# Performance work log

Hardware: AMD Instinct MI355X
Metric: run time of the kernel (lower is better)

## Reference

```python
import jax, jax.numpy as jnp
import numpy as np

B, N, D = 4, 4096, 1024       # batch, seq_len, model dim
H, DH = 16, 64                # heads, dim per head
W = 256                       # sliding window size (causal: keys in [i-W+1, i])


def setup_inputs() -> dict:
    key = jax.random.key(0)
    k1, k2, k3 = jax.random.split(key, 3)
    x = jax.random.normal(k1, (B, N, D), dtype=jnp.float32)
    w_qkv = jax.random.normal(k2, (D, 3 * H * DH), dtype=jnp.float32) * (D ** -0.5)
    w_out = jax.random.normal(k3, (H * DH, D), dtype=jnp.float32) * ((H * DH) ** -0.5)
    return {"x": x, "w_qkv": w_qkv, "w_out": w_out}


def _sliding_window_attn(q, k, v):
    """Causal sliding-window attention, banded (block-local) computation.

    q,k,v: [BH, N, DH]; query i attends keys j with i-W+1 <= j <= i.
    Identical math to masking a full NxN score matrix with -finfo.max then softmax.
    """
    BH, n, dh = q.shape
    nb = n // W  # N is a multiple of W
    qb = q.reshape(BH, nb, W, dh)
    pad = jnp.zeros((BH, W, dh), q.dtype)
    kp = jnp.concatenate([pad, k], axis=1).reshape(BH, nb + 1, W, dh)
    vp = jnp.concatenate([pad, v], axis=1).reshape(BH, nb + 1, W, dh)
    # each query block sees previous block + current block of keys -> 2W keys
    kw = jnp.concatenate([kp[:, :-1], kp[:, 1:]], axis=2)  # [BH, nb, 2W, dh]
    vw = jnp.concatenate([vp[:, :-1], vp[:, 1:]], axis=2)
    scores = jnp.einsum('bnqd,bnkd->bnqk', qb, kw)  # [BH, nb, W, 2W]
    blk = jnp.arange(nb)[:, None, None]
    ii = jnp.arange(W)[None, :, None]
    jj = jnp.arange(2 * W)[None, None, :]
    # absolute key index = blk*W + jj - W ; absolute query index = blk*W + ii
    mask = (jj - W <= ii) & (jj >= ii + 1) & (blk * W + jj - W >= 0)
    neg = -jnp.finfo(scores.dtype).max  # matches torch max_neg_value
    scores = jnp.where(mask[None], scores, neg)
    attn = jax.nn.softmax(scores, axis=-1)
    out = jnp.einsum('bnqk,bnkd->bnqd', attn, vw)
    return out.reshape(BH, n, dh)


def reference(x, w_qkv, w_out):
    b, n, d = x.shape
    qkv = x @ w_qkv                      # [b, n, 3*H*DH]
    q, k, v = jnp.split(qkv, 3, axis=-1)

    def to_heads(t):  # b n (h d) -> (b h) n d
        return t.reshape(b, n, H, DH).transpose(0, 2, 1, 3).reshape(b * H, n, DH)

    q, k, v = map(to_heads, (q, k, v))
    q = q * (DH ** -0.5)                 # default scale = dim_head**-0.5
    out = _sliding_window_attn(q, k, v)  # [(b h), n, DH]
    out = out.reshape(b, H, n, DH).transpose(0, 2, 1, 3).reshape(b, n, H * DH)
    return out @ w_out
```

## Files before the change

kernel.cpp:

```cpp
#include <hip/hip_runtime.h>

typedef __attribute__((ext_vector_type(8))) short short8;
typedef __attribute__((ext_vector_type(4))) float floatx4;

#define AS1(p) ((const __attribute__((address_space(1))) void*)(uintptr_t)(p))
#define AS3(p) ((__attribute__((address_space(3))) void*)(unsigned int)(uintptr_t)(p))

__device__ __forceinline__ unsigned short f2bf(float f) {
    union { float f; unsigned int u; } v; v.f = f;
    unsigned int u = v.u;
    unsigned int r = (u + 0x7FFFu + ((u >> 16) & 1u)) >> 16;
    return (unsigned short)r;
}

__device__ __forceinline__ int pk_bf16(float a, float b) {
#if __has_builtin(__builtin_amdgcn_cvt_pk_bf16_f32)
    auto r = __builtin_amdgcn_cvt_pk_bf16_f32(a, b);
    int out; __builtin_memcpy(&out, &r, sizeof(int)); return out;
#else
    return (int)f2bf(a) | ((int)f2bf(b) << 16);
#endif
}

__global__ __launch_bounds__(256) void transpose_bf16(const float* __restrict__ src,
                                                      unsigned short* __restrict__ dst,
                                                      int R, int C) {
    __shared__ float tile[32][33];
    int c0 = blockIdx.x * 32, r0 = blockIdx.y * 32;
    int tc = threadIdx.x & 31, tr = (threadIdx.x >> 5) * 4;
#pragma unroll
    for (int i = 0; i < 4; ++i)
        tile[tr + i][tc] = src[(size_t)(r0 + tr + i) * C + c0 + tc];
    __syncthreads();
#pragma unroll
    for (int i = 0; i < 4; ++i)
        dst[(size_t)(c0 + tr + i) * R + r0 + tc] = f2bf(tile[tc][tr + i]);
}

template <bool OUT_BF16, bool FUSE_A>
__global__ __launch_bounds__(256, 2) void gemm_bt128(const void* __restrict__ Avoid,
                                                     const unsigned short* __restrict__ Bt,
                                                     void* __restrict__ Cout,
                                                     int M, int N, int K, int nbx) {
    __shared__ unsigned short Asm[2][128 * 32];
    __shared__ unsigned short Bsm[2][256 * 32];

    const unsigned short* A16 = (const unsigned short*)Avoid;
    const float* A32 = (const float*)Avoid;

    const int tid = threadIdx.x;
    const int wn = tid >> 6, lane = tid & 63, quad = lane >> 4, l15 = lane & 15;

    const int nwg = (int)gridDim.x;
    const int q8 = nwg >> 3;
    const int wgid = (int)blockIdx.x;
    const int swz = (wgid & 7) * q8 + (wgid >> 3);
    const int bm = (swz / nbx) * 128;
    const int bn = (swz % nbx) * 256;

    floatx4 acc[8][4];
    const floatx4 z = {0.f, 0.f, 0.f, 0.f};
#pragma unroll
    for (int mi = 0; mi < 8; ++mi)
#pragma unroll
        for (int ni = 0; ni < 4; ++ni) acc[mi][ni] = z;

    const int dA0 = tid, dA1 = tid + 256;
    const int rA0 = dA0 >> 2, cA0 = ((dA0 & 3) ^ ((dA0 >> 3) & 3)) * 8;
    const int rA1 = dA1 >> 2, cA1 = ((dA1 & 3) ^ ((dA1 >> 3) & 3)) * 8;
    const unsigned short* Bsrc[4];
    int dB[4];
#pragma unroll
    for (int j = 0; j < 4; ++j) {
        dB[j] = tid + j * 256;
        const int r = dB[j] >> 2, c = ((dB[j] & 3) ^ ((dB[j] >> 3) & 3)) * 8;
        Bsrc[j] = Bt + (size_t)(bn + r) * K + c;
    }

    const int NT = K >> 5;

    auto stageB = [&](int t) {
        const int s = t & 1, ko = t * 32;
#pragma unroll
        for (int j = 0; j < 4; ++j)
            __builtin_amdgcn_global_load_lds(AS1(Bsrc[j] + ko), AS3(&Bsm[s][dB[j] * 8]), 16, 0, 0);
    };
    auto stageA16 = [&](int t) {
        const int s = t & 1, ko = t * 32;
        __builtin_amdgcn_global_load_lds(AS1(A16 + (size_t)(bm + rA0) * K + cA0 + ko),
                                         AS3(&Asm[s][dA0 * 8]), 16, 0, 0);
        __builtin_amdgcn_global_load_lds(AS1(A16 + (size_t)(bm + rA1) * K + cA1 + ko),
                                         AS3(&Asm[s][dA1 * 8]), 16, 0, 0);
    };

    float4 ar0, ar1, ar2, ar3;
    auto loadA32 = [&](int t) {
        const float* p0 = A32 + (size_t)(bm + rA0) * K + cA0 + t * 32;
        const float* p1 = A32 + (size_t)(bm + rA1) * K + cA1 + t * 32;
        ar0 = *(const float4*)p0; ar1 = *(const float4*)(p0 + 4);
        ar2 = *(const float4*)p1; ar3 = *(const float4*)(p1 + 4);
    };
    auto writeA32 = [&](int t) {
        const int s = t & 1;
        int4 w0 = {pk_bf16(ar0.x, ar0.y), pk_bf16(ar0.z, ar0.w),
                   pk_bf16(ar1.x, ar1.y), pk_bf16(ar1.z, ar1.w)};
        int4 w1 = {pk_bf16(ar2.x, ar2.y), pk_bf16(ar2.z, ar2.w),
                   pk_bf16(ar3.x, ar3.y), pk_bf16(ar3.z, ar3.w)};
        *(int4*)&Asm[s][dA0 * 8] = w0;
        *(int4*)&Asm[s][dA1 * 8] = w1;
    };

    const int qc = (quad ^ ((l15 >> 1) & 3)) * 8;
    const int brow = wn * 64 + l15;

    stageB(0);
    if (FUSE_A) { loadA32(0); writeA32(0); } else stageA16(0);
    asm volatile("s_waitcnt vmcnt(0)" ::: "memory");
    if (FUSE_A) asm volatile("s_waitcnt lgkmcnt(0)" ::: "memory");
    __builtin_amdgcn_s_barrier();

    for (int t = 0; t < NT; ++t) {
        const int s = t & 1;
        const unsigned short* Ap = Asm[s];
        const unsigned short* Bp = Bsm[s];
        if (t + 1 < NT) {
            stageB(t + 1);
            if (FUSE_A) loadA32(t + 1); else stageA16(t + 1);
        }

        short8 b[4], a0[4], a1[4];
#pragma unroll
        for (int ni = 0; ni < 4; ++ni)
            b[ni] = *(const short8*)&Bp[(brow + ni * 16) * 32 + qc];
#pragma unroll
        for (int mi = 0; mi < 4; ++mi)
            a0[mi] = *(const short8*)&Ap[(mi * 16 + l15) * 32 + qc];
#pragma unroll
        for (int mi = 0; mi < 4; ++mi)
            a1[mi] = *(const short8*)&Ap[(64 + mi * 16 + l15) * 32 + qc];

        __builtin_amdgcn_s_setprio(1);
#pragma unroll
        for (int mi = 0; mi < 4; ++mi)
#pragma unroll
            for (int ni = 0; ni < 4; ++ni)
                acc[mi][ni] = __builtin_amdgcn_mfma_f32_16x16x32_bf16(b[ni], a0[mi], acc[mi][ni], 0, 0, 0);
#pragma unroll
        for (int mi = 0; mi < 4; ++mi)
#pragma unroll
            for (int ni = 0; ni < 4; ++ni)
                acc[4 + mi][ni] = __builtin_amdgcn_mfma_f32_16x16x32_bf16(b[ni], a1[mi], acc[4 + mi][ni], 0, 0, 0);
        __builtin_amdgcn_s_setprio(0);

        if (FUSE_A && t + 1 < NT) writeA32(t + 1);
        asm volatile("s_waitcnt vmcnt(0)" ::: "memory");
        if (FUSE_A) asm volatile("s_waitcnt lgkmcnt(0)" ::: "memory");
        __builtin_amdgcn_s_barrier();
    }

#pragma unroll
    for (int mi = 0; mi < 8; ++mi) {
        const size_t row = (size_t)(bm + mi * 16 + l15);
#pragma unroll
        for (int ni = 0; ni < 4; ++ni) {
            const size_t col = (size_t)(bn + wn * 64 + ni * 16 + quad * 4);
            if (OUT_BF16) {
                int2 val = {pk_bf16(acc[mi][ni][0], acc[mi][ni][1]),
                            pk_bf16(acc[mi][ni][2], acc[mi][ni][3])};
                *(int2*)((unsigned short*)Cout + row * N + col) = val;
            } else {
                *(float4*)((float*)Cout + row * N + col) = *(const float4*)&acc[mi][ni];
            }
        }
    }
}

__global__ __launch_bounds__(256, 3) void attn_swin(const unsigned short* __restrict__ qkv,
                                                    unsigned short* __restrict__ attn_out) {
    __shared__ unsigned short Klds[2][64 * 72];
    __shared__ unsigned short Vtl[2][64 * 72];

    const int blk = blockIdx.x, bh = blockIdx.y;
    const int b = bh >> 4, h = bh & 15;
    const int tid = threadIdx.x;
    const int wave = tid >> 6, lane = tid & 63, quad = lane >> 4, l15 = lane & 15;
    const int pair = wave >> 1;
    const int qoff = (wave & 1) * 32;
    const int qi_base = blk * 128 + wave * 32;
    const size_t seqbase = (size_t)b * 4096;

    short8 qf[2][2];
#pragma unroll
    for (int qt = 0; qt < 2; ++qt)
#pragma unroll
        for (int ks = 0; ks < 2; ++ks)
            qf[qt][ks] = *(const short8*)(qkv + (seqbase + qi_base + qt * 16 + l15) * 3072
                                          + h * 64 + ks * 32 + quad * 8);

    floatx4 o[2][4];
    const floatx4 z = {0.f, 0.f, 0.f, 0.f};
    float m_run[2], l_run[2];
#pragma unroll
    for (int qt = 0; qt < 2; ++qt) {
#pragma unroll
        for (int dt = 0; dt < 4; ++dt) o[qt][dt] = z;
        m_run[qt] = -1.0e30f; l_run[qt] = 0.f;
    }

    const int kwin0 = blk * 128 - 256;
    const int c0 = (blk >= 2) ? 0 : (4 - 2 * blk);
    const int cLo = pair, cHi = pair + 4;
    const int sk_key = tid >> 2, sk_g = (tid & 3) * 16;
    const int sv_key = tid & 63, sv_dg = (tid >> 6) * 16;
    const float SC = 0.18033688f;

    const int addrA = (((quad & 1) << 5) + l15) << 2;
    const int addrB = addrA + 64;
    const bool hiq = quad >= 2;

    int4 kvreg[4];
    auto load_kv = [&](int k0) {
        const int4* sk = (const int4*)(qkv + (seqbase + k0 + sk_key) * 3072 + 1024 + h * 64 + sk_g);
        kvreg[0] = sk[0]; kvreg[1] = sk[1];
        const int4* sv = (const int4*)(qkv + (seqbase + k0 + sv_key) * 3072 + 2048 + h * 64 + sv_dg);
        kvreg[2] = sv[0]; kvreg[3] = sv[1];
    };
    auto write_kv = [&](int buf) {
        *(int4*)&Klds[buf][sk_key * 72 + sk_g]     = kvreg[0];
        *(int4*)&Klds[buf][sk_key * 72 + sk_g + 8] = kvreg[1];
        union { unsigned short s[16]; int4 q[2]; } t;
        t.q[0] = kvreg[2]; t.q[1] = kvreg[3];
#pragma unroll
        for (int i = 0; i < 16; ++i) Vtl[buf][(sv_dg + i) * 72 + sv_key] = t.s[i];
    };

    load_kv(kwin0 + c0 * 64);
    write_kv(0);

    for (int c = c0; c < 6; ++c) {
        const int buf = (c - c0) & 1;
        __syncthreads();
        if (c < 5) load_kv(kwin0 + (c + 1) * 64);

        if (c >= cLo && c <= cHi) {
            floatx4 sT[2][4];
#pragma unroll
            for (int qt = 0; qt < 2; ++qt)
#pragma unroll
                for (int ni = 0; ni < 4; ++ni) sT[qt][ni] = z;
            __builtin_amdgcn_s_setprio(1);
#pragma unroll
            for (int ks = 0; ks < 2; ++ks) {
#pragma unroll
                for (int ni = 0; ni < 4; ++ni) {
                    short8 kf = *(const short8*)&Klds[buf][(ni * 16 + l15) * 72 + ks * 32 + quad * 8];
                    sT[0][ni] = __builtin_amdgcn_mfma_f32_16x16x32_bf16(kf, qf[0][ks], sT[0][ni], 0, 0, 0);
                    sT[1][ni] = __builtin_amdgcn_mfma_f32_16x16x32_bf16(kf, qf[1][ks], sT[1][ni], 0, 0, 0);
                }
            }
            __builtin_amdgcn_s_setprio(0);

            if (c == cLo) {
#pragma unroll
                for (int qt = 0; qt < 2; ++qt) {
                    const int i64 = qoff + qt * 16 + l15;
#pragma unroll
                    for (int ni = 0; ni < 4; ++ni) {
                        int jb = ni * 16 + quad * 4;
#pragma unroll
                        for (int r = 0; r < 4; ++r)
                            if (jb + r < i64 + 1) sT[qt][ni][r] = -3.0e38f;
                    }
                }
            } else if (c == cHi) {
#pragma unroll
                for (int qt = 0; qt < 2; ++qt) {
                    const int i64 = qoff + qt * 16 + l15;
#pragma unroll
                    for (int ni = 0; ni < 4; ++ni) {
                        int jb = ni * 16 + quad * 4;
#pragma unroll
                        for (int r = 0; r < 4; ++r)
                            if (jb + r > i64) sT[qt][ni][r] = -3.0e38f;
                    }
                }
            }

            float mx[2], mn[2], alpha[2], ls[2];
            int Pk[2][4][2];
#pragma unroll
            for (int qt = 0; qt < 2; ++qt) {
                mx[qt] = -3.0e38f;
#pragma unroll
                for (int ni = 0; ni < 4; ++ni)
#pragma unroll
                    for (int r = 0; r < 4; ++r) mx[qt] = fmaxf(mx[qt], sT[qt][ni][r]);
            }
#pragma unroll
            for (int qt = 0; qt < 2; ++qt) {
                mx[qt] = fmaxf(mx[qt], __shfl_xor(mx[qt], 16));
                mx[qt] = fmaxf(mx[qt], __shfl_xor(mx[qt], 32));
                mn[qt] = fmaxf(m_run[qt], mx[qt] * SC);
                alpha[qt] = __builtin_amdgcn_exp2f(m_run[qt] - mn[qt]);
                m_run[qt] = mn[qt];
                ls[qt] = 0.f;
            }
#pragma unroll
            for (int qt = 0; qt < 2; ++qt) {
#pragma unroll
                for (int ni = 0; ni < 4; ++ni) {
                    float p0 = __builtin_amdgcn_exp2f(fmaf(sT[qt][ni][0], SC, -mn[qt]));
                    float p1 = __builtin_amdgcn_exp2f(fmaf(sT[qt][ni][1], SC, -mn[qt]));
                    float p2 = __builtin_amdgcn_exp2f(fmaf(sT[qt][ni][2], SC, -mn[qt]));
                    float p3 = __builtin_amdgcn_exp2f(fmaf(sT[qt][ni][3], SC, -mn[qt]));
                    ls[qt] += (p0 + p1) + (p2 + p3);
                    Pk[qt][ni][0] = pk_bf16(p0, p1);
                    Pk[qt][ni][1] = pk_bf16(p2, p3);
                }
            }
#pragma unroll
            for (int qt = 0; qt < 2; ++qt) {
                ls[qt] += __shfl_xor(ls[qt], 16);
                ls[qt] += __shfl_xor(ls[qt], 32);
                l_run[qt] = l_run[qt] * alpha[qt] + ls[qt];
#pragma unroll
                for (int dt = 0; dt < 4; ++dt)
#pragma unroll
                    for (int r = 0; r < 4; ++r) o[qt][dt][r] *= alpha[qt];
            }

            short8 vf[4][2];
#pragma unroll
            for (int dt = 0; dt < 4; ++dt)
#pragma unroll
                for (int ks = 0; ks < 2; ++ks)
                    vf[dt][ks] = *(const short8*)&Vtl[buf][(dt * 16 + l15) * 72 + ks * 32 + quad * 8];

#pragma unroll
            for (int qt = 0; qt < 2; ++qt) {
#pragma unroll
                for (int ks = 0; ks < 2; ++ks) {
                    int a0 = __builtin_amdgcn_ds_bpermute(addrA, Pk[qt][2 * ks][0]);
                    int b0 = __builtin_amdgcn_ds_bpermute(addrA, Pk[qt][2 * ks + 1][0]);
                    int a1 = __builtin_amdgcn_ds_bpermute(addrA, Pk[qt][2 * ks][1]);
                    int b1 = __builtin_amdgcn_ds_bpermute(addrA, Pk[qt][2 * ks + 1][1]);
                    int a2 = __builtin_amdgcn_ds_bpermute(addrB, Pk[qt][2 * ks][0]);
                    int b2 = __builtin_amdgcn_ds_bpermute(addrB, Pk[qt][2 * ks + 1][0]);
                    int a3 = __builtin_amdgcn_ds_bpermute(addrB, Pk[qt][2 * ks][1]);
                    int b3 = __builtin_amdgcn_ds_bpermute(addrB, Pk[qt][2 * ks + 1][1]);
                    union { int i[4]; short8 v; } u;
                    u.i[0] = hiq ? b0 : a0;
                    u.i[1] = hiq ? b1 : a1;
                    u.i[2] = hiq ? b2 : a2;
                    u.i[3] = hiq ? b3 : a3;
                    __builtin_amdgcn_s_setprio(1);
#pragma unroll
                    for (int dt = 0; dt < 4; ++dt)
                        o[qt][dt] = __builtin_amdgcn_mfma_f32_16x16x32_bf16(vf[dt][ks], u.v, o[qt][dt], 0, 0, 0);
                    __builtin_amdgcn_s_setprio(0);
                }
            }
        }

        if (c < 5) write_kv(buf ^ 1);
    }

#pragma unroll
    for (int qt = 0; qt < 2; ++qt) {
        float rl = __builtin_amdgcn_rcpf(l_run[qt]);
        size_t rowb = (seqbase + qi_base + qt * 16 + l15) * 1024 + h * 64;
#pragma unroll
        for (int dt = 0; dt < 4; ++dt) {
            int2 val = {pk_bf16(o[qt][dt][0] * rl, o[qt][dt][1] * rl),
                        pk_bf16(o[qt][dt][2] * rl, o[qt][dt][3] * rl)};
            *(int2*)(attn_out + rowb + dt * 16 + quad * 4) = val;
        }
    }
}

extern "C" void kernel_launch(void* const* d_in, const int* in_sizes, int n_in,
                              void* d_out, int out_size, void* d_ws, size_t ws_size,
                              hipStream_t stream) {
    const float* x     = (const float*)d_in[0];
    const float* w_qkv = (const float*)d_in[1];
    const float* w_out = (const float*)d_in[2];
    float* out = (float*)d_out;

    unsigned short* wqkvT = (unsigned short*)d_ws;
    unsigned short* woutT = wqkvT + (size_t)3072 * 1024;
    unsigned short* qkv   = woutT + (size_t)1024 * 1024;
    unsigned short* attn  = qkv   + (size_t)16384 * 3072;

    transpose_bf16<<<dim3(96, 32), 256, 0, stream>>>(w_qkv, wqkvT, 1024, 3072);
    transpose_bf16<<<dim3(32, 32), 256, 0, stream>>>(w_out, woutT, 1024, 1024);
    gemm_bt128<true, true><<<1536, 256, 0, stream>>>((const void*)x, wqkvT, qkv,
                                                     16384, 3072, 1024, 12);
    attn_swin<<<dim3(32, 64), 256, 0, stream>>>(qkv, attn);
    gemm_bt128<false, false><<<512, 256, 0, stream>>>((const void*)attn, woutT, out,
                                                      16384, 1024, 1024, 4);
}
```

Before: 395.3 us.

## Prefetch fp32 A tiles two steps ahead with ping-pong register sets

In the GEMM path that converts fp32 A to bf16 on the fly, A is now loaded into registers two K-tiles ahead, alternating between two register sets. The main loop is unrolled by two so the sets swap roles. Each step converts and writes the next tile to shared memory at the top of the step, before the MFMAs, so the latency of the global loads is hidden behind a full tile of compute. The end-of-step wait uses a partial vmcnt so the in-flight prefetch is not waited on. This adds register pressure and assumes an even tile count.

Result: faster. 381.2 us (-3.6%).

```diff
diff --git a/kernel.cpp b/kernel.cpp
--- a/kernel.cpp
+++ b/kernel.cpp
@@ -93,19 +93,24 @@
                                          AS3(&Asm[s][dA1 * 8]), 16, 0, 0);
     };
 
-    float4 ar0, ar1, ar2, ar3;
-    auto loadA32 = [&](int t) {
-        const float* p0 = A32 + (size_t)(bm + rA0) * K + cA0 + t * 32;
-        const float* p1 = A32 + (size_t)(bm + rA1) * K + cA1 + t * 32;
-        ar0 = *(const float4*)p0; ar1 = *(const float4*)(p0 + 4);
-        ar2 = *(const float4*)p1; ar3 = *(const float4*)(p1 + 4);
-    };
-    auto writeA32 = [&](int t) {
+    const float* As32_0 = FUSE_A ? A32 + (size_t)(bm + rA0) * K + cA0 : nullptr;
+    const float* As32_1 = FUSE_A ? A32 + (size_t)(bm + rA1) * K + cA1 : nullptr;
+    float4 pA0, pA1, pA2, pA3;
+    float4 pB0, pB1, pB2, pB3;
+
+    auto loadA = [&](int t, float4& r0, float4& r1, float4& r2, float4& r3) {
+        const float* p0 = As32_0 + t * 32;
+        const float* p1 = As32_1 + t * 32;
+        r0 = *(const float4*)p0; r1 = *(const float4*)(p0 + 4);
+        r2 = *(const float4*)p1; r3 = *(const float4*)(p1 + 4);
+    };
+    auto writeA = [&](int t, const float4& r0, const float4& r1,
+                      const float4& r2, const float4& r3) {
         const int s = t & 1;
-        int4 w0 = {pk_bf16(ar0.x, ar0.y), pk_bf16(ar0.z, ar0.w),
-                   pk_bf16(ar1.x, ar1.y), pk_bf16(ar1.z, ar1.w)};
-        int4 w1 = {pk_bf16(ar2.x, ar2.y), pk_bf16(ar2.z, ar2.w),
-                   pk_bf16(ar3.x, ar3.y), pk_bf16(ar3.z, ar3.w)};
+        int4 w0 = {pk_bf16(r0.x, r0.y), pk_bf16(r0.z, r0.w),
+                   pk_bf16(r1.x, r1.y), pk_bf16(r1.z, r1.w)};
+        int4 w1 = {pk_bf16(r2.x, r2.y), pk_bf16(r2.z, r2.w),
+                   pk_bf16(r3.x, r3.y), pk_bf16(r3.z, r3.w)};
         *(int4*)&Asm[s][dA0 * 8] = w0;
         *(int4*)&Asm[s][dA1 * 8] = w1;
     };
@@ -114,18 +119,32 @@
     const int brow = wn * 64 + l15;
 
     stageB(0);
-    if (FUSE_A) { loadA32(0); writeA32(0); } else stageA16(0);
-    asm volatile("s_waitcnt vmcnt(0)" ::: "memory");
-    if (FUSE_A) asm volatile("s_waitcnt lgkmcnt(0)" ::: "memory");
+    if constexpr (FUSE_A) {
+        loadA(0, pA0, pA1, pA2, pA3);
+        writeA(0, pA0, pA1, pA2, pA3);
+        if (NT > 1) loadA(1, pA0, pA1, pA2, pA3);
+        asm volatile("s_waitcnt vmcnt(4) lgkmcnt(0)" ::: "memory");
+    } else {
+        stageA16(0);
+        asm volatile("s_waitcnt vmcnt(0)" ::: "memory");
+    }
     __builtin_amdgcn_s_barrier();
 
-    for (int t = 0; t < NT; ++t) {
+    auto body = [&](int t, float4& c0r, float4& c1r, float4& c2r, float4& c3r,
+                    float4& n0r, float4& n1r, float4& n2r, float4& n3r) {
         const int s = t & 1;
         const unsigned short* Ap = Asm[s];
         const unsigned short* Bp = Bsm[s];
+        if constexpr (FUSE_A) {
+            if (t + 1 < NT)
+                writeA(t + 1, c0r, c1r, c2r, c3r);
+        }
         if (t + 1 < NT) {
             stageB(t + 1);
-            if (FUSE_A) loadA32(t + 1); else stageA16(t + 1);
+            if constexpr (!FUSE_A) stageA16(t + 1);
+        }
+        if constexpr (FUSE_A) {
+            if (t + 2 < NT) loadA(t + 2, n0r, n1r, n2r, n3r);
         }
 
         short8 b[4], a0[4], a1[4];
@@ -152,10 +171,18 @@
                 acc[4 + mi][ni] = __builtin_amdgcn_mfma_f32_16x16x32_bf16(b[ni], a1[mi], acc[4 + mi][ni], 0, 0, 0);
         __builtin_amdgcn_s_setprio(0);
 
-        if (FUSE_A && t + 1 < NT) writeA32(t + 1);
-        asm volatile("s_waitcnt vmcnt(0)" ::: "memory");
-        if (FUSE_A) asm volatile("s_waitcnt lgkmcnt(0)" ::: "memory");
+        if constexpr (FUSE_A) {
+            if (t + 2 < NT)      asm volatile("s_waitcnt vmcnt(4) lgkmcnt(0)" ::: "memory");
+            else                 asm volatile("s_waitcnt vmcnt(0) lgkmcnt(0)" ::: "memory");
+        } else {
+            asm volatile("s_waitcnt vmcnt(0)" ::: "memory");
+        }
         __builtin_amdgcn_s_barrier();
+    };
+
+    for (int tt = 0; tt < NT; tt += 2) {
+        body(tt,     pA0, pA1, pA2, pA3, pB0, pB1, pB2, pB3);
+        body(tt + 1, pB0, pB1, pB2, pB3, pA0, pA1, pA2, pA3);
     }
 
 #pragma unroll
```
